# Kernel optimization log

Hardware: AMD Instinct MI355X
Metric: run time of the kernel (lower is better)

Reference implementation:

```python
import jax, jax.numpy as jnp
import numpy as np


def setup_inputs() -> dict:
    key = jax.random.key(0)
    k1, k2, k3, k4, k5 = jax.random.split(key, 5)
    B, C, H, W = 2, 3, 64, 64
    f_tar = jax.random.normal(k1, (B, C, H, W), dtype=jnp.float32)
    f_src = jax.random.normal(k2, (B, C, H, W), dtype=jnp.float32)
    # Pinhole intrinsics (focal=50, principal point at image center) + small noise,
    # guaranteed invertible.
    K_base = jnp.array([[50.0, 0.0, 32.0], [0.0, 50.0, 32.0], [0.0, 0.0, 1.0]],
                       dtype=jnp.float32)
    K = K_base[None] + 0.05 * jax.random.normal(k3, (B, 3, 3), dtype=jnp.float32)
    # Near-identity rotation-like matrix.
    R = jnp.eye(3, dtype=jnp.float32)[None] + 0.1 * jax.random.normal(
        k4, (B, 3, 3), dtype=jnp.float32)
    t = jax.random.normal(k5, (B, 3, 1), dtype=jnp.float32)
    return {"f_tar": f_tar, "f_src": f_src, "K": K, "R": R, "t": t}


def reference(f_tar, f_src, K, R, t):
    B, C, H, W = f_src.shape  # C == 3 (required by the cross product)
    N = H * W
    dtype = f_src.dtype

    f_src_flat = f_src.reshape(B, C, N)  # (B, 3, N)
    f_tar_flat = f_tar.reshape(B, C, N)  # (B, 3, N)

    # A[b, i, j] = <f_src[:, i], f_tar[:, j]>  -> (B, N, N)
    A = jnp.einsum('bci,bcj->bij', f_src_flat, f_tar_flat)

    # Homogeneous pixel coordinates (3, N): rows of meshgrid(H, W, indexing='ij').
    ix, iy = jnp.meshgrid(jnp.arange(H), jnp.arange(W), indexing='ij')
    pix = jnp.stack([ix.reshape(-1), iy.reshape(-1), jnp.ones(N, dtype=jnp.int32)],
                    axis=0).astype(dtype)  # (3, N)

    K_inv = jnp.linalg.inv(K)  # (B, 3, 3)
    # tar_proj = K @ (R @ (K^-1 @ x) + t)   -> (B, 3, N)
    cam_rays = jnp.einsum('bij,jn->bin', K_inv, pix)
    tar_proj = jnp.einsum('bij,bjn->bin', K, jnp.einsum('bij,bjn->bin', R, cam_rays) + t)
    # Origin projects to K @ (R @ 0 + t) = K @ t, broadcast over N.
    o_proj = jnp.einsum('bij,bjn->bin', K, t)  # (B, 3, 1)

    diff = tar_proj - o_proj  # (B, 3, N)

    # Epipolar distance: || (f_src - o) x diff || / ||diff||, broadcast to (B, N, N).
    a = f_src_flat[:, :, :, None] - o_proj[:, :, :, None]  # (B, 3, N, 1)
    b = diff[:, :, None, :]                                 # (B, 3, 1, N)
    cross = jnp.cross(a, b, axis=1)                         # (B, 3, N, N)
    cross_norm = jnp.linalg.norm(cross, axis=1)             # (B, N, N)
    diff_norm = jnp.linalg.norm(diff, axis=1, keepdims=True)  # (B, 1, N)
    d_epipolar = cross_norm / diff_norm                     # (B, N, N)

    # 'sigmoid' in the original is nn.Softmax(dim=-1).
    EPI_THRESH = 0.5
    SHARPNESS = 50.0
    weight_map = 1.0 - jax.nn.softmax(SHARPNESS * (d_epipolar - EPI_THRESH), axis=-1)

    A_weighted = A * weight_map
    attention_map = jax.nn.softmax(A_weighted, axis=1)  # normalize over src positions

    # (B, N, N) @ (B, N, C) -> (B, N, C), then raw view back to (B, C, H, W)
    attended = jnp.einsum('bik,bck->bic', attention_map, f_src_flat)
    return attended.reshape(B, C, H, W)
```

## Files before the change

### kernel.cpp

```cpp
#include <hip/hip_runtime.h>

namespace {
constexpr int BB = 2;
constexpr int NN = 4096;
constexpr float LOG2E = 1.44269504088896340736f;
constexpr float T50 = 72.1347520444481703f;
constexpr float T50SQ = T50 * T50;

constexpr int OFF_W4   = 0;
constexpr int OFF_IREC = 4 * BB * NN;
constexpr int OFF_JREC = 12 * BB * NN;
constexpr int OFF_NMAX = 24 * BB * NN;
}

__device__ __forceinline__ float fsqrt(float x) { return __builtin_amdgcn_sqrtf(x); }
__device__ __forceinline__ float fexp2(float x) {
#if __has_builtin(__builtin_amdgcn_exp2f)
  return __builtin_amdgcn_exp2f(x);
#else
  return exp2f(x);
#endif
}
__device__ __forceinline__ float flog2(float x) {
#if __has_builtin(__builtin_amdgcn_logf)
  return __builtin_amdgcn_logf(x);
#else
  return log2f(x);
#endif
}

__global__ __launch_bounds__(256) void k_setup(
    const float* __restrict__ fsrc, const float* __restrict__ ftar,
    const float* __restrict__ Kb, const float* __restrict__ Rb,
    const float* __restrict__ tb, float* __restrict__ ws) {
  int gid = blockIdx.x * 256 + threadIdx.x;
  if (gid >= BB * NN) return;
  int b = gid >> 12;
  int n = gid & (NN - 1);

  float K[9], R[9], t3[3];
#pragma unroll
  for (int k = 0; k < 9; k++) { K[k] = Kb[b * 9 + k]; R[k] = Rb[b * 9 + k]; }
#pragma unroll
  for (int k = 0; k < 3; k++) t3[k] = tb[b * 3 + k];

  float c00 = K[4] * K[8] - K[5] * K[7];
  float c01 = K[5] * K[6] - K[3] * K[8];
  float c02 = K[3] * K[7] - K[4] * K[6];
  float det = K[0] * c00 + K[1] * c01 + K[2] * c02;
  float id = 1.0f / det;
  float Ki[9];
  Ki[0] = c00 * id; Ki[1] = (K[2] * K[7] - K[1] * K[8]) * id; Ki[2] = (K[1] * K[5] - K[2] * K[4]) * id;
  Ki[3] = c01 * id; Ki[4] = (K[0] * K[8] - K[2] * K[6]) * id; Ki[5] = (K[2] * K[3] - K[0] * K[5]) * id;
  Ki[6] = c02 * id; Ki[7] = (K[1] * K[6] - K[0] * K[7]) * id; Ki[8] = (K[0] * K[4] - K[1] * K[3]) * id;

  float RK[9];
#pragma unroll
  for (int i = 0; i < 3; i++)
#pragma unroll
    for (int j = 0; j < 3; j++)
      RK[i * 3 + j] = R[i * 3 + 0] * Ki[j] + R[i * 3 + 1] * Ki[3 + j] + R[i * 3 + 2] * Ki[6 + j];
  float M3[9];
#pragma unroll
  for (int i = 0; i < 3; i++)
#pragma unroll
    for (int j = 0; j < 3; j++)
      M3[i * 3 + j] = K[i * 3 + 0] * RK[j] + K[i * 3 + 1] * RK[3 + j] + K[i * 3 + 2] * RK[6 + j];
  float o0 = K[0] * t3[0] + K[1] * t3[1] + K[2] * t3[2];
  float o1 = K[3] * t3[0] + K[4] * t3[1] + K[5] * t3[2];
  float o2 = K[6] * t3[0] + K[7] * t3[1] + K[8] * t3[2];

  float sx = fsrc[b * 3 * NN + 0 * NN + n];
  float sy = fsrc[b * 3 * NN + 1 * NN + n];
  float sz = fsrc[b * 3 * NN + 2 * NN + n];
  float tx = ftar[b * 3 * NN + 0 * NN + n];
  float ty = ftar[b * 3 * NN + 1 * NN + n];
  float tz = ftar[b * 3 * NN + 2 * NN + n];

  float ux = sx - o0, uy = sy - o1, uz = sz - o2;
  float usq = ux * ux + uy * uy + uz * uz;

  float px = (float)(n >> 6), py = (float)(n & 63);
  float vx = M3[0] * px + M3[1] * py + M3[2];
  float vy = M3[3] * px + M3[4] * py + M3[5];
  float vz = M3[6] * px + M3[7] * py + M3[8];
  float invn = rsqrtf(vx * vx + vy * vy + vz * vz) * T50;
  float wx = vx * invn, wy = vy * invn, wz = vz * invn;
  float tn = fsqrt(tx * tx + ty * ty + tz * tz);

  float4* w4 = (float4*)(ws + OFF_W4);
  float4* irec = (float4*)(ws + OFF_IREC);
  float4* jrec = (float4*)(ws + OFF_JREC);
  w4[gid] = make_float4(wx, wy, wz, 0.f);
  irec[gid * 2 + 0] = make_float4(ux, uy, uz, usq * T50SQ);
  irec[gid * 2 + 1] = make_float4(sx * LOG2E, sy * LOG2E, sz * LOG2E, 0.f);
  jrec[gid * 3 + 0] = make_float4(wx, wy, wz, tn);
  jrec[gid * 3 + 1] = make_float4(tx, ty, tz, 0.f);
  jrec[gid * 3 + 2] = make_float4(sx, sy, sz, 0.f);

  float ns = fsqrt(sx * sx + sy * sy + sz * sz);
#pragma unroll
  for (int off = 32; off; off >>= 1) ns = fmaxf(ns, __shfl_xor(ns, off));
  if ((threadIdx.x & 63) == 0)
    atomicMax((unsigned int*)(ws + OFF_NMAX + b), __float_as_uint(ns));
}

__global__ __launch_bounds__(256, 4) void k_p1(float* __restrict__ ws) {
  __shared__ float sred[4][8];
  __shared__ float smax[8];
  const float4* irec = (const float4*)(ws + OFF_IREC);
  int tid = threadIdx.x, wid = tid >> 6, lane = tid & 63;
  int g0 = blockIdx.x * 8;
  int b = g0 >> 12;
  const float4* wb = (const float4*)(ws + OFF_W4) + b * NN;
  int j0 = wid * 64 + lane;

  float ux[8], uy[8], uz[8], us[8];
#pragma unroll
  for (int r = 0; r < 8; r++) {
    float4 u = irec[(g0 + r) * 2];
    ux[r] = u.x; uy[r] = u.y; uz[r] = u.z; us[r] = u.w;
  }

  float mx[8] = {0.f, 0.f, 0.f, 0.f, 0.f, 0.f, 0.f, 0.f};
  {
    float4 wc = wb[j0];
#pragma unroll
    for (int it = 0; it < 16; ++it) {
      float4 wn;
      if (it < 15) wn = wb[j0 + (it + 1) * 256];
#pragma unroll
      for (int r = 0; r < 8; r++) {
        float dot = ux[r] * wc.x + uy[r] * wc.y + uz[r] * wc.z;
        mx[r] = fmaxf(mx[r], __builtin_fmaf(-dot, dot, us[r]));
      }
      wc = wn;
    }
  }
#pragma unroll
  for (int off = 32; off; off >>= 1)
#pragma unroll
    for (int r = 0; r < 8; r++) mx[r] = fmaxf(mx[r], __shfl_xor(mx[r], off));
  if (lane == 0) {
#pragma unroll
    for (int r = 0; r < 8; r++) sred[wid][r] = mx[r];
  }
  __syncthreads();
  if (tid < 8)
    smax[tid] = fsqrt(fmaxf(fmaxf(fmaxf(sred[0][tid], sred[1][tid]),
                                  fmaxf(sred[2][tid], sred[3][tid])), 0.f));
  __syncthreads();
  float m[8];
#pragma unroll
  for (int r = 0; r < 8; r++) m[r] = smax[r];

  float s[8] = {0.f, 0.f, 0.f, 0.f, 0.f, 0.f, 0.f, 0.f};
  {
    float4 wc = wb[j0];
#pragma unroll
    for (int it = 0; it < 16; ++it) {
      float4 wn;
      if (it < 15) wn = wb[j0 + (it + 1) * 256];
#pragma unroll
      for (int r = 0; r < 8; r++) {
        float dot = ux[r] * wc.x + uy[r] * wc.y + uz[r] * wc.z;
        float d2 = fmaxf(__builtin_fmaf(-dot, dot, us[r]), 0.f);
        s[r] += fexp2(fsqrt(d2) - m[r]);
      }
      wc = wn;
    }
  }
#pragma unroll
  for (int off = 32; off; off >>= 1)
#pragma unroll
    for (int r = 0; r < 8; r++) s[r] += __shfl_xor(s[r], off);
  if (lane == 0) {
#pragma unroll
    for (int r = 0; r < 8; r++) sred[wid][r] = s[r];
  }
  __syncthreads();
  if (tid < 8) {
    float tot = sred[0][tid] + sred[1][tid] + sred[2][tid] + sred[3][tid];
    ws[OFF_IREC + (g0 + tid) * 8 + 7] = smax[tid] + flog2(tot);
  }
}

__global__ __launch_bounds__(256, 4) void k_p2(float* __restrict__ ws) {
  __shared__ float sred[4][8];
  const float4* irec = (const float4*)(ws + OFF_IREC);
  const float4* jrec = (const float4*)(ws + OFF_JREC);
  int tid = threadIdx.x, wid = tid >> 6, lane = tid & 63;
  int c0 = (blockIdx.x >> 1) * 8;
  int half = blockIdx.x & 1;
  int b = c0 >> 12;
  int base = b * NN;
  float maxns2 = ws[OFF_NMAX + b] * LOG2E;

  float wx[8], wy[8], wz[8], tx[8], ty[8], tz[8], Mb2[8];
#pragma unroll
  for (int r = 0; r < 8; r++) {
    float4 q0 = jrec[(c0 + r) * 3 + 0];
    float4 q1 = jrec[(c0 + r) * 3 + 1];
    wx[r] = q0.x; wy[r] = q0.y; wz[r] = q0.z;
    Mb2[r] = maxns2 * q0.w;
    tx[r] = q1.x; ty[r] = q1.y; tz[r] = q1.z;
  }

  float S[8] = {0.f, 0.f, 0.f, 0.f, 0.f, 0.f, 0.f, 0.f};
  int i0 = base + half * (NN / 2) + wid * 64 + lane;
  {
    float4 uc = irec[i0 * 2 + 0];
    float4 qc = irec[i0 * 2 + 1];
#pragma unroll
    for (int it = 0; it < 8; ++it) {
      float4 un, qn;
      if (it < 7) {
        int idx = i0 + (it + 1) * 256;
        un = irec[idx * 2 + 0];
        qn = irec[idx * 2 + 1];
      }
#pragma unroll
      for (int r = 0; r < 8; r++) {
        float dot = uc.x * wx[r] + uc.y * wy[r] + uc.z * wz[r];
        float d2 = fmaxf(__builtin_fmaf(-dot, dot, uc.w), 0.f);
        float en = fexp2(fsqrt(d2) - qc.w);
        float wgt = 1.f - en;
        float A2 = qc.x * tx[r] + qc.y * ty[r] + qc.z * tz[r];
        S[r] += fexp2(__builtin_fmaf(A2, wgt, -Mb2[r]));
      }
      uc = un; qc = qn;
    }
  }
#pragma unroll
  for (int off = 32; off; off >>= 1)
#pragma unroll
    for (int r = 0; r < 8; r++) S[r] += __shfl_xor(S[r], off);
  if (lane == 0) {
#pragma unroll
    for (int r = 0; r < 8; r++) sred[wid][r] = S[r];
  }
  __syncthreads();
  if (tid < 8) {
    float tot = sred[0][tid] + sred[1][tid] + sred[2][tid] + sred[3][tid];
    atomicAdd(ws + OFF_JREC + (c0 + tid) * 12 + 7, tot);
  }
}

__global__ __launch_bounds__(256, 4) void k_p3(const float* __restrict__ ws,
                                               float* __restrict__ out) {
  __shared__ float sacc[4][24];
  const float4* irec = (const float4*)(ws + OFF_IREC);
  const float4* jrec = (const float4*)(ws + OFF_JREC);
  int tid = threadIdx.x, wid = tid >> 6, lane = tid & 63;
  int g0 = (blockIdx.x >> 1) * 8;
  int half = blockIdx.x & 1;
  int b = g0 >> 12;
  int base = b * NN;
  float maxns2 = ws[OFF_NMAX + b] * LOG2E;

  float ux[8], uy[8], uz[8], us[8], ml[8], s2x[8], s2y[8], s2z[8];
#pragma unroll
  for (int r = 0; r < 8; r++) {
    float4 u = irec[(g0 + r) * 2 + 0];
    float4 sq = irec[(g0 + r) * 2 + 1];
    ux[r] = u.x; uy[r] = u.y; uz[r] = u.z; us[r] = u.w;
    s2x[r] = sq.x; s2y[r] = sq.y; s2z[r] = sq.z; ml[r] = sq.w;
  }
  float acc[8][3];
#pragma unroll
  for (int r = 0; r < 8; r++) { acc[r][0] = 0.f; acc[r][1] = 0.f; acc[r][2] = 0.f; }

  int j0 = base + half * (NN / 2) + wid * 64 + lane;
  {
    float4 q0c = jrec[j0 * 3 + 0];
    float4 q1c = jrec[j0 * 3 + 1];
    float4 q2c = jrec[j0 * 3 + 2];
#pragma unroll
    for (int it = 0; it < 8; ++it) {
      float4 q0n, q1n, q2n;
      if (it < 7) {
        int idx = j0 + (it + 1) * 256;
        q0n = jrec[idx * 3 + 0];
        q1n = jrec[idx * 3 + 1];
        q2n = jrec[idx * 3 + 2];
      }
      float cst = __builtin_fmaf(maxns2, q0c.w, flog2(q1c.w));
#pragma unroll
      for (int r = 0; r < 8; r++) {
        float dot = ux[r] * q0c.x + uy[r] * q0c.y + uz[r] * q0c.z;
        float d2 = fmaxf(__builtin_fmaf(-dot, dot, us[r]), 0.f);
        float en = fexp2(fsqrt(d2) - ml[r]);
        float wgt = 1.f - en;
        float A2 = s2x[r] * q1c.x + s2y[r] * q1c.y + s2z[r] * q1c.z;
        float p = fexp2(__builtin_fmaf(A2, wgt, -cst));
        acc[r][0] = __builtin_fmaf(p, q2c.x, acc[r][0]);
        acc[r][1] = __builtin_fmaf(p, q2c.y, acc[r][1]);
        acc[r][2] = __builtin_fmaf(p, q2c.z, acc[r][2]);
      }
      q0c = q0n; q1c = q1n; q2c = q2n;
    }
  }
#pragma unroll
  for (int off = 32; off; off >>= 1)
#pragma unroll
    for (int r = 0; r < 8; r++) {
      acc[r][0] += __shfl_xor(acc[r][0], off);
      acc[r][1] += __shfl_xor(acc[r][1], off);
      acc[r][2] += __shfl_xor(acc[r][2], off);
    }
  if (lane == 0) {
#pragma unroll
    for (int r = 0; r < 8; r++) {
      sacc[wid][r * 3 + 0] = acc[r][0];
      sacc[wid][r * 3 + 1] = acc[r][1];
      sacc[wid][r * 3 + 2] = acc[r][2];
    }
  }
  __syncthreads();
  if (tid < 24) {
    float v = sacc[0][tid] + sacc[1][tid] + sacc[2][tid] + sacc[3][tid];
    atomicAdd(out + g0 * 3 + tid, v);
  }
}

extern "C" void kernel_launch(void* const* d_in, const int* in_sizes, int n_in,
                              void* d_out, int out_size, void* d_ws, size_t ws_size,
                              hipStream_t stream) {
  (void)in_sizes; (void)n_in; (void)ws_size;
  const float* ftar = (const float*)d_in[0];
  const float* fsrc = (const float*)d_in[1];
  const float* K = (const float*)d_in[2];
  const float* R = (const float*)d_in[3];
  const float* t = (const float*)d_in[4];
  float* ws = (float*)d_ws;
  float* out = (float*)d_out;

  hipMemsetAsync((char*)d_ws + OFF_NMAX * sizeof(float), 0, BB * sizeof(float), stream);
  hipMemsetAsync(d_out, 0, out_size, stream);

  k_setup<<<dim3(32), dim3(256), 0, stream>>>(fsrc, ftar, K, R, t, ws);
  k_p1<<<dim3(1024), dim3(256), 0, stream>>>(ws);
  k_p2<<<dim3(2048), dim3(256), 0, stream>>>(ws);
  k_p3<<<dim3(2048), dim3(256), 0, stream>>>(ws, out);
}
```

Measured before the change: 127.9 us.

## Drop memsets and atomics by giving each block full rows and per-block maxima

k_setup now writes per-block norm maxima to separate slots instead of using atomicMax, and p2 reduces those 16 slots itself, which removes both memset calls. p2 and p3 each process 16 rows over the full column range per block instead of 8 rows over half the range. This allows direct stores instead of atomicAdd, and p2 now precomputes the log-sum constant that p3 previously recomputed per column. The cost is a grid of 512 blocks with more registers per thread (launch bounds lowered to 2), which could reduce occupancy and latency hiding.

```diff
diff --git a/kernel.cpp b/kernel.cpp
--- a/kernel.cpp
+++ b/kernel.cpp
@@ -33,8 +33,9 @@
     const float* __restrict__ fsrc, const float* __restrict__ ftar,
     const float* __restrict__ Kb, const float* __restrict__ Rb,
     const float* __restrict__ tb, float* __restrict__ ws) {
-  int gid = blockIdx.x * 256 + threadIdx.x;
-  if (gid >= BB * NN) return;
+  __shared__ float sm[4];
+  int tid = threadIdx.x;
+  int gid = blockIdx.x * 256 + tid;
   int b = gid >> 12;
   int n = gid & (NN - 1);
 
@@ -101,8 +102,11 @@
   float ns = fsqrt(sx * sx + sy * sy + sz * sz);
 #pragma unroll
   for (int off = 32; off; off >>= 1) ns = fmaxf(ns, __shfl_xor(ns, off));
-  if ((threadIdx.x & 63) == 0)
-    atomicMax((unsigned int*)(ws + OFF_NMAX + b), __float_as_uint(ns));
+  if ((tid & 63) == 0) sm[tid >> 6] = ns;
+  __syncthreads();
+  if (tid == 0)
+    ws[OFF_NMAX + (blockIdx.x >> 4) * 16 + (blockIdx.x & 15)] =
+        fmaxf(fmaxf(sm[0], sm[1]), fmaxf(sm[2], sm[3]));
 }
 
 __global__ __launch_bounds__(256, 4) void k_p1(float* __restrict__ ws) {
@@ -185,20 +189,23 @@
   }
 }
 
-__global__ __launch_bounds__(256, 4) void k_p2(float* __restrict__ ws) {
-  __shared__ float sred[4][8];
+__global__ __launch_bounds__(256, 2) void k_p2(float* __restrict__ ws) {
+  __shared__ float sred[4][16];
   const float4* irec = (const float4*)(ws + OFF_IREC);
   const float4* jrec = (const float4*)(ws + OFF_JREC);
   int tid = threadIdx.x, wid = tid >> 6, lane = tid & 63;
-  int c0 = (blockIdx.x >> 1) * 8;
-  int half = blockIdx.x & 1;
+  int c0 = blockIdx.x * 16;
   int b = c0 >> 12;
   int base = b * NN;
-  float maxns2 = ws[OFF_NMAX + b] * LOG2E;
-
-  float wx[8], wy[8], wz[8], tx[8], ty[8], tz[8], Mb2[8];
-#pragma unroll
-  for (int r = 0; r < 8; r++) {
+
+  float mns = ws[OFF_NMAX + b * 16];
+#pragma unroll
+  for (int k = 1; k < 16; k++) mns = fmaxf(mns, ws[OFF_NMAX + b * 16 + k]);
+  float maxns2 = mns * LOG2E;
+
+  float wx[16], wy[16], wz[16], tx[16], ty[16], tz[16], Mb2[16];
+#pragma unroll
+  for (int r = 0; r < 16; r++) {
     float4 q0 = jrec[(c0 + r) * 3 + 0];
     float4 q1 = jrec[(c0 + r) * 3 + 1];
     wx[r] = q0.x; wy[r] = q0.y; wz[r] = q0.z;
@@ -206,21 +213,23 @@
     tx[r] = q1.x; ty[r] = q1.y; tz[r] = q1.z;
   }
 
-  float S[8] = {0.f, 0.f, 0.f, 0.f, 0.f, 0.f, 0.f, 0.f};
-  int i0 = base + half * (NN / 2) + wid * 64 + lane;
+  float S[16];
+#pragma unroll
+  for (int r = 0; r < 16; r++) S[r] = 0.f;
+  int i0 = base + wid * 64 + lane;
   {
     float4 uc = irec[i0 * 2 + 0];
     float4 qc = irec[i0 * 2 + 1];
 #pragma unroll
-    for (int it = 0; it < 8; ++it) {
+    for (int it = 0; it < 16; ++it) {
       float4 un, qn;
-      if (it < 7) {
+      if (it < 15) {
         int idx = i0 + (it + 1) * 256;
         un = irec[idx * 2 + 0];
         qn = irec[idx * 2 + 1];
       }
 #pragma unroll
-      for (int r = 0; r < 8; r++) {
+      for (int r = 0; r < 16; r++) {
         float dot = uc.x * wx[r] + uc.y * wy[r] + uc.z * wz[r];
         float d2 = fmaxf(__builtin_fmaf(-dot, dot, uc.w), 0.f);
         float en = fexp2(fsqrt(d2) - qc.w);
@@ -234,65 +243,63 @@
 #pragma unroll
   for (int off = 32; off; off >>= 1)
 #pragma unroll
-    for (int r = 0; r < 8; r++) S[r] += __shfl_xor(S[r], off);
+    for (int r = 0; r < 16; r++) S[r] += __shfl_xor(S[r], off);
   if (lane == 0) {
 #pragma unroll
-    for (int r = 0; r < 8; r++) sred[wid][r] = S[r];
-  }
-  __syncthreads();
-  if (tid < 8) {
+    for (int r = 0; r < 16; r++) sred[wid][r] = S[r];
+  }
+  __syncthreads();
+  if (tid < 16) {
     float tot = sred[0][tid] + sred[1][tid] + sred[2][tid] + sred[3][tid];
-    atomicAdd(ws + OFF_JREC + (c0 + tid) * 12 + 7, tot);
-  }
-}
-
-__global__ __launch_bounds__(256, 4) void k_p3(const float* __restrict__ ws,
+    float Mb2t = maxns2 * jrec[(c0 + tid) * 3 + 0].w;
+    ws[OFF_JREC + (c0 + tid) * 12 + 7] = Mb2t + flog2(tot);
+  }
+}
+
+__global__ __launch_bounds__(256, 2) void k_p3(const float* __restrict__ ws,
                                                float* __restrict__ out) {
-  __shared__ float sacc[4][24];
+  __shared__ float sacc[4][48];
   const float4* irec = (const float4*)(ws + OFF_IREC);
   const float4* jrec = (const float4*)(ws + OFF_JREC);
   int tid = threadIdx.x, wid = tid >> 6, lane = tid & 63;
-  int g0 = (blockIdx.x >> 1) * 8;
-  int half = blockIdx.x & 1;
+  int g0 = blockIdx.x * 16;
   int b = g0 >> 12;
   int base = b * NN;
-  float maxns2 = ws[OFF_NMAX + b] * LOG2E;
-
-  float ux[8], uy[8], uz[8], us[8], ml[8], s2x[8], s2y[8], s2z[8];
-#pragma unroll
-  for (int r = 0; r < 8; r++) {
+
+  float ux[16], uy[16], uz[16], us[16], ml[16], s2x[16], s2y[16], s2z[16];
+#pragma unroll
+  for (int r = 0; r < 16; r++) {
     float4 u = irec[(g0 + r) * 2 + 0];
     float4 sq = irec[(g0 + r) * 2 + 1];
     ux[r] = u.x; uy[r] = u.y; uz[r] = u.z; us[r] = u.w;
     s2x[r] = sq.x; s2y[r] = sq.y; s2z[r] = sq.z; ml[r] = sq.w;
   }
-  float acc[8][3];
-#pragma unroll
-  for (int r = 0; r < 8; r++) { acc[r][0] = 0.f; acc[r][1] = 0.f; acc[r][2] = 0.f; }
-
-  int j0 = base + half * (NN / 2) + wid * 64 + lane;
+  float acc[16][3];
+#pragma unroll
+  for (int r = 0; r < 16; r++) { acc[r][0] = 0.f; acc[r][1] = 0.f; acc[r][2] = 0.f; }
+
+  int j0 = base + wid * 64 + lane;
   {
     float4 q0c = jrec[j0 * 3 + 0];
     float4 q1c = jrec[j0 * 3 + 1];
     float4 q2c = jrec[j0 * 3 + 2];
 #pragma unroll
-    for (int it = 0; it < 8; ++it) {
+    for (int it = 0; it < 16; ++it) {
       float4 q0n, q1n, q2n;
-      if (it < 7) {
+      if (it < 15) {
         int idx = j0 + (it + 1) * 256;
         q0n = jrec[idx * 3 + 0];
         q1n = jrec[idx * 3 + 1];
         q2n = jrec[idx * 3 + 2];
       }
-      float cst = __builtin_fmaf(maxns2, q0c.w, flog2(q1c.w));
-#pragma unroll
-      for (int r = 0; r < 8; r++) {
+#pragma unroll
+      for (int r = 0; r < 16; r++) {
         float dot = ux[r] * q0c.x + uy[r] * q0c.y + uz[r] * q0c.z;
         float d2 = fmaxf(__builtin_fmaf(-dot, dot, us[r]), 0.f);
         float en = fexp2(fsqrt(d2) - ml[r]);
         float wgt = 1.f - en;
         float A2 = s2x[r] * q1c.x + s2y[r] * q1c.y + s2z[r] * q1c.z;
-        float p = fexp2(__builtin_fmaf(A2, wgt, -cst));
+        float p = fexp2(__builtin_fmaf(A2, wgt, -q1c.w));
         acc[r][0] = __builtin_fmaf(p, q2c.x, acc[r][0]);
         acc[r][1] = __builtin_fmaf(p, q2c.y, acc[r][1]);
         acc[r][2] = __builtin_fmaf(p, q2c.z, acc[r][2]);
@@ -303,30 +310,30 @@
 #pragma unroll
   for (int off = 32; off; off >>= 1)
 #pragma unroll
-    for (int r = 0; r < 8; r++) {
+    for (int r = 0; r < 16; r++) {
       acc[r][0] += __shfl_xor(acc[r][0], off);
       acc[r][1] += __shfl_xor(acc[r][1], off);
       acc[r][2] += __shfl_xor(acc[r][2], off);
     }
   if (lane == 0) {
 #pragma unroll
-    for (int r = 0; r < 8; r++) {
+    for (int r = 0; r < 16; r++) {
       sacc[wid][r * 3 + 0] = acc[r][0];
       sacc[wid][r * 3 + 1] = acc[r][1];
       sacc[wid][r * 3 + 2] = acc[r][2];
     }
   }
   __syncthreads();
-  if (tid < 24) {
+  if (tid < 48) {
     float v = sacc[0][tid] + sacc[1][tid] + sacc[2][tid] + sacc[3][tid];
-    atomicAdd(out + g0 * 3 + tid, v);
+    out[g0 * 3 + tid] = v;
   }
 }
 
 extern "C" void kernel_launch(void* const* d_in, const int* in_sizes, int n_in,
                               void* d_out, int out_size, void* d_ws, size_t ws_size,
                               hipStream_t stream) {
-  (void)in_sizes; (void)n_in; (void)ws_size;
+  (void)in_sizes; (void)n_in; (void)out_size; (void)ws_size;
   const float* ftar = (const float*)d_in[0];
   const float* fsrc = (const float*)d_in[1];
   const float* K = (const float*)d_in[2];
@@ -335,11 +342,8 @@
   float* ws = (float*)d_ws;
   float* out = (float*)d_out;
 
-  hipMemsetAsync((char*)d_ws + OFF_NMAX * sizeof(float), 0, BB * sizeof(float), stream);
-  hipMemsetAsync(d_out, 0, out_size, stream);
-
   k_setup<<<dim3(32), dim3(256), 0, stream>>>(fsrc, ftar, K, R, t, ws);
   k_p1<<<dim3(1024), dim3(256), 0, stream>>>(ws);
-  k_p2<<<dim3(2048), dim3(256), 0, stream>>>(ws);
-  k_p3<<<dim3(2048), dim3(256), 0, stream>>>(ws, out);
-}
+  k_p2<<<dim3(512), dim3(256), 0, stream>>>(ws);
+  k_p3<<<dim3(512), dim3(256), 0, stream>>>(ws, out);
+}
```

Result: slower. 226.9 us (+77.4%).
